# Kernel optimization log

Measured on AMD Instinct MI355X. Metric: run time of the kernel, lower is better.

## Reference

```python
import jax, jax.numpy as jnp
import numpy as np

B, T, D_IN, H, D = 4, 4096, 1024, 16, 64


def setup_inputs() -> dict:
    key = jax.random.key(0)
    k1, k2, k3 = jax.random.split(key, 3)
    inputs = jax.random.normal(k1, (B, T, D_IN), dtype=jnp.float32)
    kv_kernel = jax.random.normal(k2, (D_IN, H, D, 2), dtype=jnp.float32) * (1.0 / np.sqrt(D_IN))
    q_kernel = jax.random.normal(k3, (H, D), dtype=jnp.float32) * (1.0 / np.sqrt(D))
    return {"inputs": inputs, "kv_kernel": kv_kernel, "q_kernel": q_kernel}


def _associate(a, b):
    # Online-softmax combine on packed tuples [m(1), u(1), w(D)] along last axis.
    ma, ua, wa = a[..., :1], a[..., 1:2], a[..., 2:]
    mb, ub, wb = b[..., :1], b[..., 1:2], b[..., 2:]
    m = jnp.maximum(ma, mb)
    ea = jnp.exp(ma - m)
    eb = jnp.exp(mb - m)
    u = ua * ea + ub * eb
    w = wa * ea + wb * eb
    return jnp.concatenate([m, u, w], axis=-1)


def reference(inputs, kv_kernel, q_kernel):
    # inputs: (B,T,D_in); kv_kernel: (D_in,H,D,2); q_kernel: (H,D)
    kv = jnp.einsum('bti,ihdk->bthdk', inputs, kv_kernel)
    kv = jax.nn.relu(kv)  # activation; dropout disabled (inference)
    k = kv[..., 0]  # (B,T,H,D)
    v = kv[..., 1]  # (B,T,H,D)
    st = jnp.einsum('hd,bthd->bth', q_kernel, k)[..., None]  # (B,T,H,1)
    u_init = jnp.ones_like(st)  # exp(s - m) with m = s
    elems = jnp.concatenate([st, u_init, v], axis=-1)  # (B,T,H,D+2)
    o = jax.lax.associative_scan(_associate, elems, axis=1)
    c = o[..., 1:2]  # running denominator
    a = o[..., 2:]   # running numerator (B,T,H,D)
    h = a / c
    # concat_heads=False -> sum over heads
    return jnp.sum(h, axis=-2)  # (B,T,D)
```

## Files before the change

kernel.cpp:

```cpp
#include <hip/hip_runtime.h>
#include <hip/hip_bf16.h>
#include <math.h>

#define B_   4
#define T_   4096
#define DIN_ 1024
#define H_   16
#define D_   64
#define M_   (B_*T_)
#define N_   (H_*D_*2)
#define K_   DIN_
#define C_   64
#define CL_  (T_/C_)

typedef unsigned short u16;
typedef __attribute__((ext_vector_type(8))) short short8_t;
typedef __attribute__((ext_vector_type(4))) float float4_t;

__device__ __forceinline__ u16 f2bf(float f) {
  unsigned int x = __float_as_uint(f);
  x += 0x7fffu + ((x >> 16) & 1u);
  return (u16)(x >> 16);
}
__device__ __forceinline__ float bf2f(unsigned int u) {
  return __uint_as_float((u & 0xffffu) << 16);
}

__device__ __forceinline__ void g2l16(const u16* g, u16* l) {
  __builtin_amdgcn_global_load_lds(
      (const __attribute__((address_space(1))) void*)g,
      (__attribute__((address_space(3))) void*)l, 16, 0, 0);
}

__global__ __launch_bounds__(256)
void prep(const float* __restrict__ inputs, const float* __restrict__ kvk,
          u16* __restrict__ aB, u16* __restrict__ wBt) {
  __shared__ float tile[32][33];
  int bid = blockIdx.x;
  int tid = threadIdx.x;
  if (bid < 8192) {
    int i = bid * 256 + tid;
    const float4* src = (const float4*)inputs;
    float4 a = src[2*i], b = src[2*i+1];
    uint4 o;
    o.x = (unsigned)f2bf(a.x) | ((unsigned)f2bf(a.y) << 16);
    o.y = (unsigned)f2bf(a.z) | ((unsigned)f2bf(a.w) << 16);
    o.z = (unsigned)f2bf(b.x) | ((unsigned)f2bf(b.y) << 16);
    o.w = (unsigned)f2bf(b.z) | ((unsigned)f2bf(b.w) << 16);
    ((uint4*)aB)[i] = o;
  } else {
    int b2 = bid - 8192;
    int kb = (b2 & 31) * 32;
    int nb = (b2 >> 5) * 32;
    int r  = tid >> 3;
    int c4 = (tid & 7) * 4;
    float4 v = *(const float4*)&kvk[(size_t)(kb + r) * N_ + nb + c4];
    tile[r][c4+0] = v.x; tile[r][c4+1] = v.y; tile[r][c4+2] = v.z; tile[r][c4+3] = v.w;
    __syncthreads();
    unsigned lo = (unsigned)f2bf(tile[c4+0][r]) | ((unsigned)f2bf(tile[c4+1][r]) << 16);
    unsigned hi = (unsigned)f2bf(tile[c4+2][r]) | ((unsigned)f2bf(tile[c4+3][r]) << 16);
    uint2 o; o.x = lo; o.y = hi;
    *(uint2*)&wBt[(size_t)(nb + r) * K_ + kb + c4] = o;
  }
}

__global__ __launch_bounds__(256)
void gemm_kv(const u16* __restrict__ A, const u16* __restrict__ Bt,
             u16* __restrict__ kbuf, u16* __restrict__ vbuf) {
  __shared__ u16 lA[128][32];
  __shared__ u16 lB[128][32];
  const int tid  = threadIdx.x;
  const int wave = tid >> 6;
  const int lane = tid & 63;
  const int quad = lane >> 4;
  const int l16  = lane & 15;
  const int bm = blockIdx.x * 128;
  const int bn = blockIdx.y * 128;
  const int wm = (wave >> 1) * 64;
  const int wn = (wave & 1) * 64;

  const int r4 = lane >> 2;
  const int cc = lane & 3;
  const int gk = ((cc ^ ((r4 >> 1) & 3))) * 8;
  const u16* ga0 = A  + (size_t)(bm + wave*16 + r4) * K_ + gk;
  const u16* ga1 = ga0 + (size_t)64 * K_;
  const u16* gb0 = Bt + (size_t)(bn + wave*16 + r4) * K_ + gk;
  const u16* gb1 = gb0 + (size_t)64 * K_;
  u16* la0 = &lA[wave*16][0];
  u16* la1 = &lA[64 + wave*16][0];
  u16* lb0 = &lB[wave*16][0];
  u16* lb1 = &lB[64 + wave*16][0];

  const int swz = (quad ^ ((l16 >> 1) & 3)) * 8;

  float4_t acc[4][4] = {};

  for (int k0 = 0; k0 < K_; k0 += 32) {
    __syncthreads();
    g2l16(ga0 + k0, la0);
    g2l16(ga1 + k0, la1);
    g2l16(gb0 + k0, lb0);
    g2l16(gb1 + k0, lb1);
    __syncthreads();

    short8_t af[4], bfr[4];
#pragma unroll
    for (int i = 0; i < 4; ++i)
      af[i] = *(const short8_t*)&lA[wm + i*16 + l16][swz];
#pragma unroll
    for (int j = 0; j < 4; ++j)
      bfr[j] = *(const short8_t*)&lB[wn + j*16 + l16][swz];
#pragma unroll
    for (int i = 0; i < 4; ++i)
#pragma unroll
      for (int j = 0; j < 4; ++j)
        acc[i][j] = __builtin_amdgcn_mfma_f32_16x16x32_bf16(af[i], bfr[j], acc[i][j], 0, 0, 0);
  }

#pragma unroll
  for (int j = 0; j < 4; ++j) {
    int n   = bn + wn + j*16 + l16;
    int h   = n >> 7;
    int rem = n & 127;
    int d   = rem >> 1;
    bool isv = (rem & 1) != 0;
#pragma unroll
    for (int i = 0; i < 4; ++i) {
#pragma unroll
      for (int r = 0; r < 4; ++r) {
        int m = bm + wm + i*16 + quad*4 + r;
        float val = acc[i][j][r];
        val = val > 0.f ? val : 0.f;
        size_t kidx = (size_t)m * (H_*D_) + h * D_ + d;
        size_t vidx = (((size_t)(m >> 12) * H_ + h) * T_ + (m & (T_-1))) * D_ + d;
        u16* dst = isv ? vbuf : kbuf;
        dst[isv ? vidx : kidx] = f2bf(val);
      }
    }
  }
}

__global__ __launch_bounds__(64)
void scan_pass1(const u16* __restrict__ kbuf, const u16* __restrict__ vbuf,
                const float* __restrict__ q,
                float* __restrict__ aggM, float* __restrict__ aggU,
                float* __restrict__ aggW) {
  __shared__ float sS[CL_];
  int blk = blockIdx.x;
  int bh  = blk >> 6;
  int c   = blk & (C_ - 1);
  int b   = bh >> 4, h = bh & 15;
  int t0  = c * CL_;
  int tid = threadIdx.x;

  const u16*  kr = kbuf + ((size_t)(b * T_ + t0 + tid) * H_ + h) * D_;
  const float* qr = q + h * D_;
  float s = 0.f;
#pragma unroll
  for (int j = 0; j < 8; ++j) {
    uint4 kp = *(const uint4*)(kr + j*8);
    float4 qa = *(const float4*)(qr + j*8);
    float4 qb = *(const float4*)(qr + j*8 + 4);
    s += bf2f(kp.x) * qa.x + bf2f(kp.x >> 16) * qa.y;
    s += bf2f(kp.y) * qa.z + bf2f(kp.y >> 16) * qa.w;
    s += bf2f(kp.z) * qb.x + bf2f(kp.z >> 16) * qb.y;
    s += bf2f(kp.w) * qb.z + bf2f(kp.w >> 16) * qb.w;
  }
  sS[tid] = s;
  __syncthreads();

  int d = tid;
  const u16* vp = vbuf + ((size_t)bh * T_ + t0) * D_ + d;
  float m = -INFINITY, u = 0.f, w = 0.f;
#pragma unroll 4
  for (int i = 0; i < CL_; ++i) {
    float si = sS[i];
    float v  = bf2f(vp[i * D_]);
    float mn    = fmaxf(m, si);
    float alpha = __expf(m - mn);
    float p     = __expf(si - mn);
    u = u * alpha + p;
    w = w * alpha + p * v;
    m = mn;
  }
  aggW[(size_t)blk * D_ + d] = w;
  if (d == 0) { aggM[blk] = m; aggU[blk] = u; }
}

__global__ __launch_bounds__(1024)
void scan_pass3(const u16* __restrict__ kbuf, const u16* __restrict__ vbuf,
                const float* __restrict__ q,
                const float* __restrict__ aggM, const float* __restrict__ aggU,
                const float* __restrict__ aggW, float* __restrict__ out) {
  __shared__ float sS[H_][CL_];
  __shared__ float wbuf[H_][8][D_ + 1];
  int bc = blockIdx.x;
  int b  = bc >> 6;
  int c  = bc & (C_ - 1);
  int tid  = threadIdx.x;
  int h    = tid >> 6;
  int lane = tid & 63;
  int bh   = b * H_ + h;
  int t0   = c * CL_;

  const u16*  kr = kbuf + ((size_t)(b * T_ + t0 + lane) * H_ + h) * D_;
  const float* qr = q + h * D_;
  float s = 0.f;
#pragma unroll
  for (int j = 0; j < 8; ++j) {
    uint4 kp = *(const uint4*)(kr + j*8);
    float4 qa = *(const float4*)(qr + j*8);
    float4 qb = *(const float4*)(qr + j*8 + 4);
    s += bf2f(kp.x) * qa.x + bf2f(kp.x >> 16) * qa.y;
    s += bf2f(kp.y) * qa.z + bf2f(kp.y >> 16) * qa.w;
    s += bf2f(kp.z) * qb.x + bf2f(kp.z >> 16) * qb.y;
    s += bf2f(kp.w) * qb.z + bf2f(kp.w >> 16) * qb.w;
  }
  sS[h][lane] = s;

  float m = -INFINITY, u = 0.f, w = 0.f;
  for (int j = 0; j < c; ++j) {
    int idx = bh * C_ + j;
    float Mc = aggM[idx];
    float Uc = aggU[idx];
    float Wc = aggW[(size_t)idx * D_ + lane];
    float mn = fmaxf(m, Mc);
    float ea = __expf(m - mn);
    float eb = __expf(Mc - mn);
    u = u * ea + Uc * eb;
    w = w * ea + Wc * eb;
    m = mn;
  }
  __syncthreads();

  const u16* vp = vbuf + ((size_t)bh * T_ + t0) * D_ + lane;
  for (int g = 0; g < 8; ++g) {
#pragma unroll
    for (int ii = 0; ii < 8; ++ii) {
      int i = g * 8 + ii;
      float si = sS[h][i];
      float v  = bf2f(vp[i * D_]);
      float mn    = fmaxf(m, si);
      float alpha = __expf(m - mn);
      float p     = __expf(si - mn);
      u = u * alpha + p;
      w = w * alpha + p * v;
      m = mn;
      wbuf[h][ii][lane] = __fdividef(w, u);
    }
    __syncthreads();
    if (tid < 512) {
      int ii = tid >> 6, dd = tid & 63;
      float acc = 0.f;
#pragma unroll
      for (int hh = 0; hh < H_; ++hh) acc += wbuf[hh][ii][dd];
      out[((size_t)b * T_ + t0 + g*8 + ii) * D_ + dd] = acc;
    }
    __syncthreads();
  }
}

extern "C" void kernel_launch(void* const* d_in, const int* in_sizes, int n_in,
                              void* d_out, int out_size, void* d_ws, size_t ws_size,
                              hipStream_t stream) {
  const float* inputs = (const float*)d_in[0];
  const float* kvk    = (const float*)d_in[1];
  const float* qk     = (const float*)d_in[2];
  float* out = (float*)d_out;
  char* ws = (char*)d_ws;

  u16*   aB   = (u16*)ws;
  u16*   wBt  = (u16*)(ws + 33554432);
  u16*   kb   = (u16*)(ws + 37748736);
  u16*   vb   = (u16*)(ws + 71303168);
  float* aggM = (float*)(ws + 104857600);
  float* aggU = (float*)(ws + 104873984);
  float* aggW = (float*)(ws + 104890368);

  prep<<<10240, 256, 0, stream>>>(inputs, kvk, aB, wBt);
  gemm_kv<<<dim3(M_/128, N_/128), 256, 0, stream>>>(aB, wBt, kb, vb);
  scan_pass1<<<B_*H_*C_, 64, 0, stream>>>(kb, vb, qk, aggM, aggU, aggW);
  scan_pass3<<<B_*C_, 1024, 0, stream>>>(kb, vb, qk, aggM, aggU, aggW, out);
}
```

Measured before the change: 249.0 us.

## Fuse score dot-product into GEMM epilogue and stage V stores through LDS

The GEMM epilogue now computes the per-token score q·relu(k) directly from the accumulators, reducing across lanes through shared memory, and writes only a float score buffer instead of the full bf16 K tensor. V tiles are staged in LDS and written out with coalesced 16-byte stores in head-major layout. The grid is reordered so each block owns one head's 128 columns. This removes the K write and the two K re-reads in the scan kernels, in exchange for extra LDS usage and synchronisation in the GEMM epilogue.

Measured after the change: 236.9 us. 4.8% less time.

```diff
diff --git a/kernel.cpp b/kernel.cpp
--- a/kernel.cpp
+++ b/kernel.cpp
@@ -66,18 +66,28 @@
 
 __global__ __launch_bounds__(256)
 void gemm_kv(const u16* __restrict__ A, const u16* __restrict__ Bt,
-             u16* __restrict__ kbuf, u16* __restrict__ vbuf) {
-  __shared__ u16 lA[128][32];
-  __shared__ u16 lB[128][32];
+             const float* __restrict__ q,
+             float* __restrict__ sbuf, u16* __restrict__ vbuf) {
+  __shared__ __align__(16) char smem[27136];
+  u16*   lA    = (u16*)smem;
+  u16*   lB    = (u16*)(smem + 8192);
+  u16*   vtile = (u16*)smem;
+  float* sred  = (float*)(smem + 18432);
+  __shared__ float qs[D_];
+
   const int tid  = threadIdx.x;
   const int wave = tid >> 6;
   const int lane = tid & 63;
   const int quad = lane >> 4;
   const int l16  = lane & 15;
-  const int bm = blockIdx.x * 128;
-  const int bn = blockIdx.y * 128;
+  const int h    = blockIdx.x;
+  const int mt   = blockIdx.y;
+  const int bm = mt * 128;
+  const int bn = h * 128;
   const int wm = (wave >> 1) * 64;
   const int wn = (wave & 1) * 64;
+
+  if (tid < D_) qs[tid] = q[h * D_ + tid];
 
   const int r4 = lane >> 2;
   const int cc = lane & 3;
@@ -86,10 +96,10 @@
   const u16* ga1 = ga0 + (size_t)64 * K_;
   const u16* gb0 = Bt + (size_t)(bn + wave*16 + r4) * K_ + gk;
   const u16* gb1 = gb0 + (size_t)64 * K_;
-  u16* la0 = &lA[wave*16][0];
-  u16* la1 = &lA[64 + wave*16][0];
-  u16* lb0 = &lB[wave*16][0];
-  u16* lb1 = &lB[64 + wave*16][0];
+  u16* la0 = lA + (wave*16) * 32;
+  u16* la1 = lA + (64 + wave*16) * 32;
+  u16* lb0 = lB + (wave*16) * 32;
+  u16* lb1 = lB + (64 + wave*16) * 32;
 
   const int swz = (quad ^ ((l16 >> 1) & 3)) * 8;
 
@@ -106,10 +116,10 @@
     short8_t af[4], bfr[4];
 #pragma unroll
     for (int i = 0; i < 4; ++i)
-      af[i] = *(const short8_t*)&lA[wm + i*16 + l16][swz];
+      af[i] = *(const short8_t*)&lA[(wm + i*16 + l16) * 32 + swz];
 #pragma unroll
     for (int j = 0; j < 4; ++j)
-      bfr[j] = *(const short8_t*)&lB[wn + j*16 + l16][swz];
+      bfr[j] = *(const short8_t*)&lB[(wn + j*16 + l16) * 32 + swz];
 #pragma unroll
     for (int i = 0; i < 4; ++i)
 #pragma unroll
@@ -117,56 +127,72 @@
         acc[i][j] = __builtin_amdgcn_mfma_f32_16x16x32_bf16(af[i], bfr[j], acc[i][j], 0, 0, 0);
   }
 
-#pragma unroll
-  for (int j = 0; j < 4; ++j) {
-    int n   = bn + wn + j*16 + l16;
-    int h   = n >> 7;
-    int rem = n & 127;
-    int d   = rem >> 1;
-    bool isv = (rem & 1) != 0;
-#pragma unroll
-    for (int i = 0; i < 4; ++i) {
+  __syncthreads();
+
+  if (l16 & 1) {
+#pragma unroll
+    for (int j = 0; j < 4; ++j) {
+      int d = ((wn + j*16 + l16) & 127) >> 1;
+#pragma unroll
+      for (int i = 0; i < 4; ++i)
+#pragma unroll
+        for (int r = 0; r < 4; ++r) {
+          int t = wm + i*16 + quad*4 + r;
+          vtile[t*72 + d] = f2bf(fmaxf(acc[i][j][r], 0.f));
+        }
+    }
+  } else {
+    int slot = (wn >> 3) + (l16 >> 1);
+#pragma unroll
+    for (int i = 0; i < 4; ++i)
 #pragma unroll
       for (int r = 0; r < 4; ++r) {
-        int m = bm + wm + i*16 + quad*4 + r;
-        float val = acc[i][j][r];
-        val = val > 0.f ? val : 0.f;
-        size_t kidx = (size_t)m * (H_*D_) + h * D_ + d;
-        size_t vidx = (((size_t)(m >> 12) * H_ + h) * T_ + (m & (T_-1))) * D_ + d;
-        u16* dst = isv ? vbuf : kbuf;
-        dst[isv ? vidx : kidx] = f2bf(val);
+        int t = wm + i*16 + quad*4 + r;
+        float p = 0.f;
+#pragma unroll
+        for (int j = 0; j < 4; ++j) {
+          int d = ((wn + j*16 + l16) & 127) >> 1;
+          p += qs[d] * fmaxf(acc[i][j][r], 0.f);
+        }
+        sred[t*17 + slot] = p;
       }
-    }
+  }
+  __syncthreads();
+
+  const int b  = mt >> 5;
+  const int t0 = (mt & 31) * 128;
+
+  {
+    int tr = tid >> 3;
+    int d0 = (tid & 7) * 8;
+    u16* vg = vbuf + ((size_t)(b * H_ + h) * T_ + t0) * D_;
+#pragma unroll
+    for (int it = 0; it < 4; ++it) {
+      int t = tr + 32*it;
+      uint4 val = *(const uint4*)&vtile[t*72 + d0];
+      *(uint4*)&vg[(size_t)t * D_ + d0] = val;
+    }
+  }
+  if (tid < 128) {
+    float ssum = 0.f;
+#pragma unroll
+    for (int k = 0; k < 16; ++k) ssum += sred[tid*17 + k];
+    sbuf[(size_t)(b * H_ + h) * T_ + t0 + tid] = ssum;
   }
 }
 
 __global__ __launch_bounds__(64)
-void scan_pass1(const u16* __restrict__ kbuf, const u16* __restrict__ vbuf,
-                const float* __restrict__ q,
+void scan_pass1(const u16* __restrict__ vbuf, const float* __restrict__ sbuf,
                 float* __restrict__ aggM, float* __restrict__ aggU,
                 float* __restrict__ aggW) {
   __shared__ float sS[CL_];
   int blk = blockIdx.x;
   int bh  = blk >> 6;
   int c   = blk & (C_ - 1);
-  int b   = bh >> 4, h = bh & 15;
   int t0  = c * CL_;
   int tid = threadIdx.x;
 
-  const u16*  kr = kbuf + ((size_t)(b * T_ + t0 + tid) * H_ + h) * D_;
-  const float* qr = q + h * D_;
-  float s = 0.f;
-#pragma unroll
-  for (int j = 0; j < 8; ++j) {
-    uint4 kp = *(const uint4*)(kr + j*8);
-    float4 qa = *(const float4*)(qr + j*8);
-    float4 qb = *(const float4*)(qr + j*8 + 4);
-    s += bf2f(kp.x) * qa.x + bf2f(kp.x >> 16) * qa.y;
-    s += bf2f(kp.y) * qa.z + bf2f(kp.y >> 16) * qa.w;
-    s += bf2f(kp.z) * qb.x + bf2f(kp.z >> 16) * qb.y;
-    s += bf2f(kp.w) * qb.z + bf2f(kp.w >> 16) * qb.w;
-  }
-  sS[tid] = s;
+  sS[tid] = sbuf[(size_t)bh * T_ + t0 + tid];
   __syncthreads();
 
   int d = tid;
@@ -188,8 +214,7 @@
 }
 
 __global__ __launch_bounds__(1024)
-void scan_pass3(const u16* __restrict__ kbuf, const u16* __restrict__ vbuf,
-                const float* __restrict__ q,
+void scan_pass3(const u16* __restrict__ vbuf, const float* __restrict__ sbuf,
                 const float* __restrict__ aggM, const float* __restrict__ aggU,
                 const float* __restrict__ aggW, float* __restrict__ out) {
   __shared__ float sS[H_][CL_];
@@ -203,20 +228,7 @@
   int bh   = b * H_ + h;
   int t0   = c * CL_;
 
-  const u16*  kr = kbuf + ((size_t)(b * T_ + t0 + lane) * H_ + h) * D_;
-  const float* qr = q + h * D_;
-  float s = 0.f;
-#pragma unroll
-  for (int j = 0; j < 8; ++j) {
-    uint4 kp = *(const uint4*)(kr + j*8);
-    float4 qa = *(const float4*)(qr + j*8);
-    float4 qb = *(const float4*)(qr + j*8 + 4);
-    s += bf2f(kp.x) * qa.x + bf2f(kp.x >> 16) * qa.y;
-    s += bf2f(kp.y) * qa.z + bf2f(kp.y >> 16) * qa.w;
-    s += bf2f(kp.z) * qb.x + bf2f(kp.z >> 16) * qb.y;
-    s += bf2f(kp.w) * qb.z + bf2f(kp.w >> 16) * qb.w;
-  }
-  sS[h][lane] = s;
+  sS[h][lane] = sbuf[(size_t)bh * T_ + t0 + lane];
 
   float m = -INFINITY, u = 0.f, w = 0.f;
   for (int j = 0; j < c; ++j) {
@@ -271,14 +283,14 @@
 
   u16*   aB   = (u16*)ws;
   u16*   wBt  = (u16*)(ws + 33554432);
-  u16*   kb   = (u16*)(ws + 37748736);
-  u16*   vb   = (u16*)(ws + 71303168);
-  float* aggM = (float*)(ws + 104857600);
-  float* aggU = (float*)(ws + 104873984);
-  float* aggW = (float*)(ws + 104890368);
+  u16*   vb   = (u16*)(ws + 37748736);
+  float* sb   = (float*)(ws + 71303168);
+  float* aggM = (float*)(ws + 72351744);
+  float* aggU = (float*)(ws + 72368128);
+  float* aggW = (float*)(ws + 72384512);
 
   prep<<<10240, 256, 0, stream>>>(inputs, kvk, aB, wBt);
-  gemm_kv<<<dim3(M_/128, N_/128), 256, 0, stream>>>(aB, wBt, kb, vb);
-  scan_pass1<<<B_*H_*C_, 64, 0, stream>>>(kb, vb, qk, aggM, aggU, aggW);
-  scan_pass3<<<B_*C_, 1024, 0, stream>>>(kb, vb, qk, aggM, aggU, aggW, out);
-}
+  gemm_kv<<<dim3(H_, M_/128), 256, 0, stream>>>(aB, wBt, qk, sb, vb);
+  scan_pass1<<<B_*H_*C_, 64, 0, stream>>>(vb, sb, aggM, aggU, aggW);
+  scan_pass3<<<B_*C_, 1024, 0, stream>>>(vb, sb, aggM, aggU, aggW, out);
+}
```
